# Performance work log

Measured on AMD Instinct MI355X. Metric: run time of the kernel, lower is better.

Reference implementation:

```python
import jax, jax.numpy as jnp
import numpy as np

N, E, B = 100000, 160000, 4096
F_NODE, F_EDGE, H, DEPTH = 133, 14, 512, 5


def setup_inputs() -> dict:
    key = jax.random.key(0)
    ks = jax.random.split(key, 12)
    P = E // 2
    src = jax.random.randint(ks[0], (P,), 0, N)
    dst = jax.random.randint(ks[1], (P,), 0, N)
    # interleave so edge 2k = (src,dst) and 2k+1 = (dst,src); reverse of e is e^1
    row = jnp.stack([src, dst], axis=1).reshape(-1)
    col = jnp.stack([dst, src], axis=1).reshape(-1)
    edge_index = jnp.stack([row, col], axis=0)
    x = jax.random.normal(ks[2], (N, F_NODE), jnp.float32)
    edge_attr = jax.random.normal(ks[3], (E, F_EDGE), jnp.float32)
    batch = jnp.sort(jax.random.randint(ks[4], (N,), 0, B))
    s = 0.05
    return dict(
        x=x, edge_attr=edge_attr, edge_index=edge_index, batch=batch,
        W_init=jax.random.normal(ks[5], (F_NODE + F_EDGE, H), jnp.float32) * s,
        b_init=jnp.zeros((H,), jnp.float32),
        W_conv=jax.random.normal(ks[6], (DEPTH, H, H), jnp.float32) * s,
        b_conv=jnp.zeros((DEPTH, H), jnp.float32),
        W_e2n=jax.random.normal(ks[7], (F_NODE + H, H), jnp.float32) * s,
        b_e2n=jnp.zeros((H,), jnp.float32),
        W_ffn1=jax.random.normal(ks[8], (H, H), jnp.float32) * s,
        b_ffn1=jnp.zeros((H,), jnp.float32),
        W_ffn2=jax.random.normal(ks[9], (H, 1), jnp.float32) * s,
        b_ffn2=jnp.zeros((1,), jnp.float32),
    )


def _dmpnn_conv(h, row, col, rev, W, b):
    # node aggregation: sum incoming edge messages at each destination node
    a = jax.ops.segment_sum(h, col, num_segments=N)          # [N, H]
    # new edge message for (i->j): agg at i minus reverse-edge message (j->i)
    msg = a[row] - h[rev]                                    # [E, H]
    return a, msg @ W + b


def reference(x, edge_attr, edge_index, batch, W_init, b_init, W_conv, b_conv,
              W_e2n, b_e2n, W_ffn1, b_ffn1, W_ffn2, b_ffn2):
    row, col = edge_index[0], edge_index[1]
    rev = jnp.arange(E) ^ 1
    # edge_init: relu(Linear(cat([x[row], edge_attr])))
    h0 = jax.nn.relu(jnp.concatenate([x[row], edge_attr], axis=1) @ W_init + b_init)
    h = h0
    for l in range(DEPTH):
        _, h = _dmpnn_conv(h, row, col, rev, W_conv[l], b_conv[l])
        h = jax.nn.relu(h + h0)  # residual to h0, relu (dropout=0, eval mode)
    # final conv reuses last layer (l == DEPTH-1 as in the torch loop variable)
    s_node, _ = _dmpnn_conv(h, row, col, rev, W_conv[DEPTH - 1], b_conv[DEPTH - 1])
    q = jnp.concatenate([x, s_node], axis=1)                 # [N, F_NODE+H]
    hn = jax.nn.relu(q @ W_e2n + b_e2n)                      # [N, H]
    pooled = jax.ops.segment_sum(hn, batch, num_segments=B)  # global_add_pool [B, H]
    out = jax.nn.relu(pooled @ W_ffn1 + b_ffn1) @ W_ffn2 + b_ffn2
    return out.squeeze(-1)                                   # [B]
```

## Files before the change

### kernel.cpp

```cpp
#include <hip/hip_runtime.h>

typedef _Float16 f16;
typedef _Float16 f16x8 __attribute__((ext_vector_type(8)));
typedef float f32x4 __attribute__((ext_vector_type(4)));

#define NN 100000
#define NE 160000
#define NB 4096
#define HD 512

#define O_H8    0UL
#define O_SCE   81920000UL
#define O_SHR   87040000UL
#define O_WT    141440000UL
#define O_OFF   145437696UL
#define O_EID   145837712UL
#define WS_NEEDED 146477712UL
#define V_POOL  0UL
#define V_PH    8388608UL
#define V_T1    12582912UL
#define V_CNT   16777216UL
#define V_FILL  17177232UL
#define V_BSUM  17577248UL

__global__ void zero16(ulong2* __restrict__ p, long n) {
  long i = (long)blockIdx.x * 256 + threadIdx.x;
  if (i < n) p[i] = ulong2{0UL, 0UL};
}
__global__ void diag(float* __restrict__ out, int n, float v) {
  int i = blockIdx.x * 256 + threadIdx.x;
  if (i < n) out[i] = v;
}

__global__ void transcast(const float* __restrict__ src, f16* __restrict__ dst,
                          int Kreal, int Kpad) {
  int id = blockIdx.x * 256 + threadIdx.x;
  if (id >= 512 * Kpad) return;
  int n = id / Kpad, k = id % Kpad;
  dst[((k >> 5) * 512 + n) * 32 + (k & 31)] =
      (k < Kreal) ? (f16)src[(size_t)k * 512 + n] : (f16)0.f;
}

__global__ void countK(const int* __restrict__ col, int* __restrict__ cnt) {
  int e = blockIdx.x * 256 + threadIdx.x;
  if (e < NE) atomicAdd(&cnt[col[e]], 1);
}
__global__ __launch_bounds__(1024) void scanA(const int* __restrict__ cnt,
                                              int* __restrict__ incl, int* __restrict__ bsum) {
  __shared__ int s[1024];
  int i = blockIdx.x * 1024 + threadIdx.x;
  s[threadIdx.x] = (i < NN) ? cnt[i] : 0;
  __syncthreads();
  for (int d = 1; d < 1024; d <<= 1) {
    int t = (threadIdx.x >= d) ? s[threadIdx.x - d] : 0;
    __syncthreads();
    s[threadIdx.x] += t;
    __syncthreads();
  }
  if (i < NN) incl[i] = s[threadIdx.x];
  if (threadIdx.x == 1023) bsum[blockIdx.x] = s[1023];
}
__global__ void scanB(int* bsum, int nb) {
  if (threadIdx.x == 0 && blockIdx.x == 0) {
    int run = 0;
    for (int i = 0; i < nb; ++i) { int t = bsum[i]; bsum[i] = run; run += t; }
  }
}
__global__ __launch_bounds__(1024) void scanC(const int* __restrict__ cnt,
                                              int* __restrict__ incl_fill,
                                              const int* __restrict__ bsum,
                                              int* __restrict__ off) {
  int i = blockIdx.x * 1024 + threadIdx.x;
  if (i >= NN) return;
  int g = incl_fill[i] + bsum[blockIdx.x];
  off[i + 1] = g;
  incl_fill[i] = g - cnt[i];
  if (i == 0) off[0] = 0;
}
__global__ void scatterK(const int* __restrict__ col, int* __restrict__ fill,
                         int* __restrict__ eid) {
  int e = blockIdx.x * 256 + threadIdx.x;
  if (e >= NE) return;
  int p = atomicAdd(&fill[col[e]], 1);
  eid[p] = e;
}

template<int C0>
__global__ __launch_bounds__(256, 4)
void msgk(const char* __restrict__ z8, const float* __restrict__ sce,
          const int* __restrict__ off, const int* __restrict__ eid,
          char* __restrict__ msgq, float* __restrict__ scm) {
  int tid = threadIdx.x, wid = tid >> 6, lane = tid & 63;
  int n = blockIdx.x * 4 + wid;
  int s0 = off[n], s1 = off[n + 1];
  int g = lane >> 4;
  float a[4] = {0.f, 0.f, 0.f, 0.f};
  for (int p = s0; p < s1; ++p) {
    int e = eid[p];
    float sc = sce[e * 8 + (C0 >> 6) + g];
    unsigned u = *reinterpret_cast<const unsigned*>(z8 + (size_t)e * 512 + C0 + lane * 4);
    #pragma unroll
    for (int b = 0; b < 4; ++b)
      a[b] += (float)(char)((u >> (8 * b)) & 0xff) * sc;
  }
  for (int p = s0; p < s1; ++p) {
    int e = eid[p];
    int f = e ^ 1;
    float sc = sce[e * 8 + (C0 >> 6) + g];
    unsigned u = *reinterpret_cast<const unsigned*>(z8 + (size_t)e * 512 + C0 + lane * 4);
    float mv[4]; float m = 0.f;
    #pragma unroll
    for (int b = 0; b < 4; ++b) {
      mv[b] = a[b] - (float)(char)((u >> (8 * b)) & 0xff) * sc;
      m = fmaxf(m, fabsf(mv[b]));
    }
    #pragma unroll
    for (int d = 1; d < 16; d <<= 1) m = fmaxf(m, __shfl_xor(m, d));
    float s2 = (m > 0.f) ? m / 127.f : 1.f;
    if ((lane & 15) == 0) scm[f * 4 + g] = s2;
    unsigned q = 0;
    #pragma unroll
    for (int b = 0; b < 4; ++b) {
      int qi = __float2int_rn(mv[b] / s2);
      qi = min(127, max(-127, qi));
      q |= ((unsigned)(unsigned char)(char)qi) << (8 * b);
    }
    *reinterpret_cast<unsigned*>(msgq + (size_t)f * 256 + lane * 4) = q;
  }
}

__global__ __launch_bounds__(256, 4)
void tker(const char* __restrict__ h8, const float* __restrict__ sce,
          const int* __restrict__ off, const int* __restrict__ eid,
          char* __restrict__ nb8, float* __restrict__ scn) {
  int tid = threadIdx.x, wid = tid >> 6, lane = tid & 63;
  int n = blockIdx.x * 4 + wid;
  int s0 = off[n], s1 = off[n + 1];
  int g = lane >> 3;
  float a[8] = {0.f,0.f,0.f,0.f,0.f,0.f,0.f,0.f};
  for (int p = s0; p < s1; ++p) {
    int e = eid[p];
    float sc = sce[e * 8 + g];
    uint2 u = *reinterpret_cast<const uint2*>(h8 + (size_t)e * 512 + lane * 8);
    #pragma unroll
    for (int b = 0; b < 4; ++b) {
      a[b]     += (float)((u.x >> (8 * b)) & 0xff) * sc;
      a[4 + b] += (float)((u.y >> (8 * b)) & 0xff) * sc;
    }
  }
  float m = 0.f;
  #pragma unroll
  for (int j = 0; j < 8; ++j) m = fmaxf(m, a[j]);
  #pragma unroll
  for (int d = 1; d < 8; d <<= 1) m = fmaxf(m, __shfl_xor(m, d));
  float s2 = (m > 0.f) ? m / 255.f : 1.f;
  if ((lane & 7) == 0) scn[n * 8 + g] = s2;
  unsigned lo = 0, hi = 0;
  #pragma unroll
  for (int b = 0; b < 4; ++b) {
    int q0 = __float2int_rn(a[b] / s2);     q0 = min(255, max(0, q0));
    int q1 = __float2int_rn(a[4 + b] / s2); q1 = min(255, max(0, q1));
    lo |= ((unsigned)q0) << (8 * b);
    hi |= ((unsigned)q1) << (8 * b);
  }
  *reinterpret_cast<uint2*>(nb8 + (size_t)n * 512 + lane * 8) = uint2{lo, hi};
}

static __device__ __forceinline__ void stageB512(const f16* __restrict__ wsrc,
                                                 f16* __restrict__ Bs, int tid) {
  #pragma unroll
  for (int j = 0; j < 4; ++j) {
    int u = tid * 4 + j;
    *reinterpret_cast<f16x8*>(&Bs[(u >> 2) * 40 + (u & 3) * 8]) =
        *reinterpret_cast<const f16x8*>(&wsrc[u * 8]);
  }
}
template<int AS>
static __device__ __forceinline__ void mstep8(const f16* __restrict__ As,
                                              const f16* __restrict__ Bs,
                                              f32x4 acc[2][8], int wm, int wn,
                                              int fr, int fg, int ko) {
  f16x8 af[2];
  #pragma unroll
  for (int mf = 0; mf < 2; ++mf)
    af[mf] = *reinterpret_cast<const f16x8*>(&As[(wm + mf * 16 + fr) * AS + ko + fg * 8]);
  #pragma unroll
  for (int nf = 0; nf < 8; ++nf) {
    f16x8 bf = *reinterpret_cast<const f16x8*>(&Bs[(wn + nf * 16 + fr) * 40 + fg * 8]);
    #pragma unroll
    for (int mf = 0; mf < 2; ++mf)
      acc[mf][nf] = __builtin_amdgcn_mfma_f32_16x16x32_f16(af[mf], bf, acc[mf][nf], 0, 0, 0);
  }
}

__global__ __launch_bounds__(512, 1)
void zk(char* __restrict__ h8, float* __restrict__ sce, const f16* __restrict__ wst) {
  __shared__ f16 As[64 * 520];
  __shared__ f16 Bs[2][512 * 40];
  const int tid = threadIdx.x, lane = tid & 63, wid = tid >> 6;
  const int fr = lane & 15, fg = lane >> 4;
  const int wm = (wid >> 2) * 32, wn = (wid & 3) * 128;
  const int e0 = blockIdx.x * 64;

  {
    int r = tid >> 3, s = tid & 7, kb = s * 64;
    float sc = sce[(size_t)(e0 + r) * 8 + s];
    const int4* src = reinterpret_cast<const int4*>(h8 + (size_t)(e0 + r) * 512 + kb);
    #pragma unroll
    for (int j = 0; j < 4; ++j) {
      int4 w = src[j];
      unsigned vv[4] = {(unsigned)w.x, (unsigned)w.y, (unsigned)w.z, (unsigned)w.w};
      f16 tmp[16];
      #pragma unroll
      for (int q = 0; q < 4; ++q)
        #pragma unroll
        for (int b = 0; b < 4; ++b)
          tmp[q * 4 + b] = (f16)((float)((vv[q] >> (8 * b)) & 0xff) * sc);
      *reinterpret_cast<f16x8*>(&As[r * 520 + kb + j * 16])     = *reinterpret_cast<f16x8*>(&tmp[0]);
      *reinterpret_cast<f16x8*>(&As[r * 520 + kb + j * 16 + 8]) = *reinterpret_cast<f16x8*>(&tmp[8]);
    }
  }
  stageB512(wst, Bs[0], tid);
  __syncthreads();
  f32x4 acc[2][8] = {};
  for (int step = 0; step < 16; ++step) {
    const int cur = step & 1;
    f16x8 pf[4];
    if (step < 15) {
      const f16* wsrc = wst + (size_t)(step + 1) * 16384;
      #pragma unroll
      for (int j = 0; j < 4; ++j)
        pf[j] = *reinterpret_cast<const f16x8*>(&wsrc[(size_t)(tid * 4 + j) * 8]);
    }
    mstep8<520>(As, Bs[cur], acc, wm, wn, fr, fg, step * 32);
    if (step < 15) {
      #pragma unroll
      for (int j = 0; j < 4; ++j) {
        int u = tid * 4 + j;
        *reinterpret_cast<f16x8*>(&Bs[cur ^ 1][(u >> 2) * 40 + (u & 3) * 8]) = pf[j];
      }
    }
    __syncthreads();
  }
  float scA[2][4], scB[2][4];
  #pragma unroll
  for (int mf = 0; mf < 2; ++mf)
    #pragma unroll
    for (int i = 0; i < 4; ++i) {
      float mA = 0.f, mB = 0.f;
      #pragma unroll
      for (int nf = 0; nf < 4; ++nf) mA = fmaxf(mA, fabsf(acc[mf][nf][i]));
      #pragma unroll
      for (int nf = 4; nf < 8; ++nf) mB = fmaxf(mB, fabsf(acc[mf][nf][i]));
      #pragma unroll
      for (int d = 1; d < 16; d <<= 1) {
        mA = fmaxf(mA, __shfl_xor(mA, d));
        mB = fmaxf(mB, __shfl_xor(mB, d));
      }
      scA[mf][i] = (mA > 0.f) ? mA / 127.f : 1.f;
      scB[mf][i] = (mB > 0.f) ? mB / 127.f : 1.f;
      if (fr == 0) {
        int r = wm + mf * 16 + fg * 4 + i;
        sce[(size_t)(e0 + r) * 8 + (wn >> 6)]     = scA[mf][i];
        sce[(size_t)(e0 + r) * 8 + (wn >> 6) + 1] = scB[mf][i];
      }
    }
  char* q8 = (char*)&Bs[0][0];
  #pragma unroll
  for (int mf = 0; mf < 2; ++mf)
    #pragma unroll
    for (int nf = 0; nf < 8; ++nf) {
      int c = wn + nf * 16 + fr;
      #pragma unroll
      for (int i = 0; i < 4; ++i) {
        int r = wm + mf * 16 + fg * 4 + i;
        float s = (nf < 4) ? scA[mf][i] : scB[mf][i];
        int q = __float2int_rn(acc[mf][nf][i] / s);
        q8[r * 512 + c] = (char)min(127, max(-127, q));
      }
    }
  __syncthreads();
  { int4* dst = reinterpret_cast<int4*>(h8 + (size_t)e0 * 512);
    const int4* s4 = reinterpret_cast<const int4*>(q8);
    #pragma unroll
    for (int j = 0; j < 4; ++j) dst[tid * 4 + j] = s4[tid * 4 + j]; }
}

template<int MODE>
__global__ __launch_bounds__(512, 2)
void convup(const float* __restrict__ x, const float* __restrict__ ea,
            const int* __restrict__ row, const f16* __restrict__ wi,
            const float* __restrict__ bi, const float* __restrict__ bc,
            char* __restrict__ h8, float* __restrict__ sce,
            const char* __restrict__ msgq, const float* __restrict__ scm,
            int c0) {
  __shared__ f16 As[64 * 168];
  __shared__ f16 Bs[2][256 * 40];
  __shared__ char m8s[64 * 256];
  __shared__ float scmL[64 * 4];
  const int tid = threadIdx.x, lane = tid & 63, wid = tid >> 6;
  const int fr = lane & 15, fg = lane >> 4;
  const int wm = (wid >> 2) * 32, wn = (wid & 3) * 64;
  const int e0 = blockIdx.x * 64;

  {
    int r = tid >> 3, s = tid & 7;
    int rid = row[e0 + r];
    for (int k = s; k < 133; k += 8) As[r * 168 + k] = (f16)x[(size_t)rid * 133 + k];
    for (int k = 133 + s; k < 147; k += 8) As[r * 168 + k] = (f16)ea[(size_t)(e0 + r) * 14 + (k - 133)];
    for (int k = 147 + s; k < 160; k += 8) As[r * 168 + k] = (f16)0.f;
    if (MODE == 1) {
      const int4* ms = reinterpret_cast<const int4*>(msgq + (size_t)(e0 + r) * 256 + s * 32);
      int4* md = reinterpret_cast<int4*>(m8s + r * 256 + s * 32);
      md[0] = ms[0]; md[1] = ms[1];
      if (s < 4) scmL[r * 4 + s] = scm[(size_t)(e0 + r) * 4 + s];
    }
  }
  {
    #pragma unroll
    for (int j = 0; j < 2; ++j) {
      int u = tid * 2 + j;
      *reinterpret_cast<f16x8*>(&Bs[0][(u >> 2) * 40 + (u & 3) * 8]) =
          *reinterpret_cast<const f16x8*>(&wi[(size_t)c0 * 32 + (size_t)u * 8]);
    }
  }
  __syncthreads();
  f32x4 acc[2][4] = {};
  for (int step = 0; step < 5; ++step) {
    const int cur = step & 1;
    f16x8 pf[2];
    if (step < 4) {
      const f16* wsrc = wi + (size_t)(step + 1) * 16384 + (size_t)c0 * 32;
      #pragma unroll
      for (int j = 0; j < 2; ++j)
        pf[j] = *reinterpret_cast<const f16x8*>(&wsrc[(size_t)(tid * 2 + j) * 8]);
    }
    f16x8 af[2];
    #pragma unroll
    for (int mf = 0; mf < 2; ++mf)
      af[mf] = *reinterpret_cast<const f16x8*>(&As[(wm + mf * 16 + fr) * 168 + step * 32 + fg * 8]);
    #pragma unroll
    for (int nf = 0; nf < 4; ++nf) {
      f16x8 bf = *reinterpret_cast<const f16x8*>(&Bs[cur][(wn + nf * 16 + fr) * 40 + fg * 8]);
      #pragma unroll
      for (int mf = 0; mf < 2; ++mf)
        acc[mf][nf] = __builtin_amdgcn_mfma_f32_16x16x32_f16(af[mf], bf, acc[mf][nf], 0, 0, 0);
    }
    if (step < 4) {
      #pragma unroll
      for (int j = 0; j < 2; ++j) {
        int u = tid * 2 + j;
        *reinterpret_cast<f16x8*>(&Bs[cur ^ 1][(u >> 2) * 40 + (u & 3) * 8]) = pf[j];
      }
    }
    __syncthreads();
  }
  #pragma unroll
  for (int nf = 0; nf < 4; ++nf) {
    int cl = wn + nf * 16 + fr;
    int cg = c0 + cl;
    float bi_ = bi[cg];
    float bc_ = (MODE == 1) ? bc[cg] : 0.f;
    #pragma unroll
    for (int mf = 0; mf < 2; ++mf)
      #pragma unroll
      for (int i = 0; i < 4; ++i) {
        int r = wm + mf * 16 + fg * 4 + i;
        float v = fmaxf(acc[mf][nf][i] + bi_, 0.f);
        if (MODE == 1) {
          float mv = (float)(char)m8s[r * 256 + cl] * scmL[r * 4 + (cl >> 6)];
          v = fmaxf(v + bc_ + mv, 0.f);
        }
        acc[mf][nf][i] = v;
      }
  }
  float sc_[2][4];
  #pragma unroll
  for (int mf = 0; mf < 2; ++mf)
    #pragma unroll
    for (int i = 0; i < 4; ++i) {
      float m = 0.f;
      #pragma unroll
      for (int nf = 0; nf < 4; ++nf) m = fmaxf(m, acc[mf][nf][i]);
      #pragma unroll
      for (int d = 1; d < 16; d <<= 1) m = fmaxf(m, __shfl_xor(m, d));
      sc_[mf][i] = (m > 0.f) ? m / 255.f : 1.f;
      if (fr == 0)
        sce[(size_t)(e0 + wm + mf * 16 + fg * 4 + i) * 8 + (c0 >> 6) + (wn >> 6)] = sc_[mf][i];
    }
  __syncthreads();
  #pragma unroll
  for (int mf = 0; mf < 2; ++mf)
    #pragma unroll
    for (int nf = 0; nf < 4; ++nf) {
      int cl = wn + nf * 16 + fr;
      #pragma unroll
      for (int i = 0; i < 4; ++i) {
        int r = wm + mf * 16 + fg * 4 + i;
        int q = __float2int_rn(acc[mf][nf][i] / sc_[mf][i]);
        m8s[r * 256 + cl] = (char)(unsigned char)min(255, max(0, q));
      }
    }
  __syncthreads();
  { int r = tid >> 3, s = tid & 7;
    int4* dst = reinterpret_cast<int4*>(h8 + (size_t)(e0 + r) * 512 + c0 + s * 32);
    const int4* sp = reinterpret_cast<const int4*>(m8s + r * 256 + s * 32);
    dst[0] = sp[0]; dst[1] = sp[1]; }
}

__global__ __launch_bounds__(512, 1)
void e2n(const float* __restrict__ x, const char* __restrict__ nb8,
         const float* __restrict__ scn, const f16* __restrict__ wex,
         const f16* __restrict__ wes, const float* __restrict__ be,
         const int* __restrict__ batch, float* __restrict__ pooled) {
  __shared__ f16 As[64 * 520];
  __shared__ f16 Bs[2][512 * 40];
  __shared__ int bat[64];
  const int tid = threadIdx.x, lane = tid & 63, wid = tid >> 6;
  const int fr = lane & 15, fg = lane >> 4;
  const int wm = (wid >> 2) * 32, wn = (wid & 3) * 128;
  const int n0 = blockIdx.x * 64;
  if (tid < 64) { int nn = n0 + tid; bat[tid] = (nn < NN) ? batch[nn] : 0; }
  {
    int r = tid >> 3, s = tid & 7;
    int nid = min(n0 + r, NN - 1);
    for (int k = s; k < 133; k += 8) As[r * 168 + k] = (f16)x[(size_t)nid * 133 + k];
    for (int k = 133 + s; k < 160; k += 8) As[r * 168 + k] = (f16)0.f;
  }
  stageB512(wex, Bs[0], tid);
  __syncthreads();
  f32x4 acc[2][8] = {};
  for (int step = 0; step < 5; ++step) {
    const int cur = step & 1;
    f16x8 pf[4];
    if (step < 4) {
      const f16* wsrc = wex + (size_t)(step + 1) * 16384;
      #pragma unroll
      for (int j = 0; j < 4; ++j)
        pf[j] = *reinterpret_cast<const f16x8*>(&wsrc[(size_t)(tid * 4 + j) * 8]);
    }
    mstep8<168>(As, Bs[cur], acc, wm, wn, fr, fg, step * 32);
    if (step < 4) {
      #pragma unroll
      for (int j = 0; j < 4; ++j) {
        int u = tid * 4 + j;
        *reinterpret_cast<f16x8*>(&Bs[cur ^ 1][(u >> 2) * 40 + (u & 3) * 8]) = pf[j];
      }
    }
    __syncthreads();
  }
  {
    int r = tid >> 3, s = tid & 7, kb = s * 64;
    int nid = min(n0 + r, NN - 1);
    float sc = scn[(size_t)nid * 8 + s];
    const int4* src = reinterpret_cast<const int4*>(nb8 + (size_t)nid * 512 + kb);
    #pragma unroll
    for (int j = 0; j < 4; ++j) {
      int4 w = src[j];
      unsigned vv[4] = {(unsigned)w.x, (unsigned)w.y, (unsigned)w.z, (unsigned)w.w};
      f16 tmp[16];
      #pragma unroll
      for (int q = 0; q < 4; ++q)
        #pragma unroll
        for (int b = 0; b < 4; ++b)
          tmp[q * 4 + b] = (f16)((float)((vv[q] >> (8 * b)) & 0xff) * sc);
      *reinterpret_cast<f16x8*>(&As[r * 520 + kb + j * 16])     = *reinterpret_cast<f16x8*>(&tmp[0]);
      *reinterpret_cast<f16x8*>(&As[r * 520 + kb + j * 16 + 8]) = *reinterpret_cast<f16x8*>(&tmp[8]);
    }
  }
  stageB512(wes, Bs[0], tid);
  __syncthreads();
  for (int step = 0; step < 16; ++step) {
    const int cur = step & 1;
    f16x8 pf[4];
    if (step < 15) {
      const f16* wsrc = wes + (size_t)(step + 1) * 16384;
      #pragma unroll
      for (int j = 0; j < 4; ++j)
        pf[j] = *reinterpret_cast<const f16x8*>(&wsrc[(size_t)(tid * 4 + j) * 8]);
    }
    mstep8<520>(As, Bs[cur], acc, wm, wn, fr, fg, step * 32);
    if (step < 15) {
      #pragma unroll
      for (int j = 0; j < 4; ++j) {
        int u = tid * 4 + j;
        *reinterpret_cast<f16x8*>(&Bs[cur ^ 1][(u >> 2) * 40 + (u & 3) * 8]) = pf[j];
      }
    }
    __syncthreads();
  }
  #pragma unroll
  for (int nf = 0; nf < 8; ++nf) {
    int c = wn + nf * 16 + fr;
    float b_ = be[c];
    #pragma unroll
    for (int mf = 0; mf < 2; ++mf)
      #pragma unroll
      for (int i = 0; i < 4; ++i) {
        int rl = wm + mf * 16 + fg * 4 + i;
        As[rl * 520 + c] = (f16)fmaxf(acc[mf][nf][i] + b_, 0.f);
      }
  }
  __syncthreads();
  {
    const int c = tid;
    float s = 0.f;
    int pb = bat[0];
    #pragma unroll 1
    for (int r = 0; r < 64; ++r) {
      if (n0 + r >= NN) break;
      int b = bat[r];
      if (b != pb) {
        atomicAdd(&pooled[(size_t)pb * 512 + c], s);
        s = 0.f; pb = b;
      }
      s += (float)As[r * 520 + c];
    }
    atomicAdd(&pooled[(size_t)pb * 512 + c], s);
  }
}

__global__ __launch_bounds__(512, 1)
void ffn1(const f16* __restrict__ ph, const f16* __restrict__ wf,
          const float* __restrict__ b1, f16* __restrict__ t1) {
  __shared__ f16 As[64 * 520];
  __shared__ f16 Bs[2][512 * 40];
  const int tid = threadIdx.x, lane = tid & 63, wid = tid >> 6;
  const int fr = lane & 15, fg = lane >> 4;
  const int wm = (wid >> 2) * 32, wn = (wid & 3) * 128;
  const int n0 = blockIdx.x * 64;
  { int r = tid >> 3, hs = (tid & 7) * 64;
    #pragma unroll
    for (int j = 0; j < 8; ++j)
      *reinterpret_cast<f16x8*>(&As[r * 520 + hs + j * 8]) =
          *reinterpret_cast<const f16x8*>(&ph[(size_t)(n0 + r) * 512 + hs + j * 8]); }
  stageB512(wf, Bs[0], tid);
  __syncthreads();
  f32x4 acc[2][8] = {};
  for (int step = 0; step < 16; ++step) {
    const int cur = step & 1;
    f16x8 pf[4];
    if (step < 15) {
      const f16* wsrc = wf + (size_t)(step + 1) * 16384;
      #pragma unroll
      for (int j = 0; j < 4; ++j)
        pf[j] = *reinterpret_cast<const f16x8*>(&wsrc[(size_t)(tid * 4 + j) * 8]);
    }
    mstep8<520>(As, Bs[cur], acc, wm, wn, fr, fg, step * 32);
    if (step < 15) {
      #pragma unroll
      for (int j = 0; j < 4; ++j) {
        int u = tid * 4 + j;
        *reinterpret_cast<f16x8*>(&Bs[cur ^ 1][(u >> 2) * 40 + (u & 3) * 8]) = pf[j];
      }
    }
    __syncthreads();
  }
  f16* q16 = As;
  #pragma unroll
  for (int nf = 0; nf < 8; ++nf) {
    int c = wn + nf * 16 + fr;
    float b_ = b1[c];
    #pragma unroll
    for (int mf = 0; mf < 2; ++mf)
      #pragma unroll
      for (int i = 0; i < 4; ++i) {
        int r = wm + mf * 16 + fg * 4 + i;
        q16[r * 512 + c] = (f16)fmaxf(acc[mf][nf][i] + b_, 0.f);
      }
  }
  __syncthreads();
  #pragma unroll
  for (int j = 0; j < 8; ++j)
    *reinterpret_cast<f16x8*>(&t1[(size_t)n0 * 512 + tid * 64 + j * 8]) =
        *reinterpret_cast<const f16x8*>(&q16[tid * 64 + j * 8]);
}

__global__ void cast_ph(const float* __restrict__ pooled, f16* __restrict__ ph) {
  int id = blockIdx.x * 256 + threadIdx.x;
  if (id >= NB * 64) return;
  int k = id * 8;
  f16 v[8];
  #pragma unroll
  for (int i = 0; i < 8; ++i) v[i] = (f16)pooled[k + i];
  *reinterpret_cast<f16x8*>(&ph[k]) = *reinterpret_cast<f16x8*>(&v[0]);
}

__global__ void final_out(const f16* __restrict__ t, const float* __restrict__ W2,
                          const float* __restrict__ b2, float* __restrict__ out) {
  int id = blockIdx.x * 256 + threadIdx.x;
  if (id >= NB * 64) return;
  int b = id >> 6, lane = id & 63;
  f16x8 v = *reinterpret_cast<const f16x8*>(&t[(size_t)b * HD + lane * 8]);
  float s = 0.f;
  #pragma unroll
  for (int i = 0; i < 8; ++i) s += (float)v[i] * W2[lane * 8 + i];
  #pragma unroll
  for (int o = 32; o > 0; o >>= 1) s += __shfl_down(s, o);
  if (lane == 0) out[b] = s + b2[0];
}

extern "C" void kernel_launch(void* const* d_in, const int* in_sizes, int n_in,
                              void* d_out, int out_size, void* d_ws, size_t ws_size,
                              hipStream_t stream) {
  const float* x      = (const float*)d_in[0];
  const float* ea     = (const float*)d_in[1];
  const int*   ei     = (const int*)d_in[2];
  const int*   batch  = (const int*)d_in[3];
  const float* W_init = (const float*)d_in[4];
  const float* b_init = (const float*)d_in[5];
  const float* W_conv = (const float*)d_in[6];
  const float* b_conv = (const float*)d_in[7];
  const float* W_e2n  = (const float*)d_in[8];
  const float* b_e2n  = (const float*)d_in[9];
  const float* W_ffn1 = (const float*)d_in[10];
  const float* b_ffn1 = (const float*)d_in[11];
  const float* W_ffn2 = (const float*)d_in[12];
  const float* b_ffn2 = (const float*)d_in[13];
  const int* row = ei;
  const int* col = ei + NE;
  float* out = (float*)d_out;

  if (ws_size < WS_NEEDED) {
    diag<<<(out_size + 255) / 256, 256, 0, stream>>>(out, out_size, (float)(ws_size >> 20));
    return;
  }

  char* ws = (char*)d_ws;
  char*  h8   = ws + O_H8;
  float* sce  = (float*)(ws + O_SCE);
  char*  msgq = ws + O_SHR;
  float* scm  = (float*)(ws + O_SHR + 40960000UL);
  char*  nb8  = ws + O_SHR;
  float* scn  = (float*)(ws + O_SHR + 51200000UL);
  f16*   wt   = (f16*)(ws + O_WT);
  int*   off  = (int*)(ws + O_OFF);
  int*   eid  = (int*)(ws + O_EID);
  float* pooled = (float*)(ws + V_POOL);
  f16*   ph   = (f16*)(ws + V_PH);
  f16*   t1   = (f16*)(ws + V_T1);
  int*   cnt  = (int*)(ws + V_CNT);
  int*   fill = (int*)(ws + V_FILL);
  int*   bsum = (int*)(ws + V_BSUM);

  f16* wi  = wt;
  f16* wc  = wi + 160 * 512;
  f16* wex = wc + 5 * 512 * 512;
  f16* wes = wex + 160 * 512;
  f16* wf1 = wes + 512 * 512;

  transcast<<<(512 * 160 + 255) / 256, 256, 0, stream>>>(W_init, wi, 147, 160);
  for (int l = 0; l < 5; ++l)
    transcast<<<(512 * 512 + 255) / 256, 256, 0, stream>>>(
        W_conv + (size_t)l * 262144, wc + (size_t)l * 262144, 512, 512);
  transcast<<<(512 * 160 + 255) / 256, 256, 0, stream>>>(W_e2n, wex, 133, 160);
  transcast<<<(512 * 512 + 255) / 256, 256, 0, stream>>>(W_e2n + 133 * 512, wes, 512, 512);
  transcast<<<(512 * 512 + 255) / 256, 256, 0, stream>>>(W_ffn1, wf1, 512, 512);

  zero16<<<(25000 + 255) / 256, 256, 0, stream>>>((ulong2*)cnt, 25000);
  countK<<<(NE + 255) / 256, 256, 0, stream>>>(col, cnt);
  scanA<<<98, 1024, 0, stream>>>(cnt, fill, bsum);
  scanB<<<1, 64, 0, stream>>>(bsum, 98);
  scanC<<<98, 1024, 0, stream>>>(cnt, fill, bsum, off);
  scatterK<<<(NE + 255) / 256, 256, 0, stream>>>(col, fill, eid);

  convup<0><<<2500, 512, 0, stream>>>(x, ea, row, wi, b_init, nullptr,
                                      h8, sce, nullptr, nullptr, 0);
  convup<0><<<2500, 512, 0, stream>>>(x, ea, row, wi, b_init, nullptr,
                                      h8, sce, nullptr, nullptr, 256);
  for (int l = 0; l < 5; ++l) {
    zk<<<2500, 512, 0, stream>>>(h8, sce, wc + (size_t)l * 262144);
    msgk<0><<<25000, 256, 0, stream>>>(h8, sce, off, eid, msgq, scm);
    convup<1><<<2500, 512, 0, stream>>>(x, ea, row, wi, b_init, b_conv + l * 512,
                                        h8, sce, msgq, scm, 0);
    msgk<256><<<25000, 256, 0, stream>>>(h8, sce, off, eid, msgq, scm);
    convup<1><<<2500, 512, 0, stream>>>(x, ea, row, wi, b_init, b_conv + l * 512,
                                        h8, sce, msgq, scm, 256);
  }
  tker<<<25000, 256, 0, stream>>>(h8, sce, off, eid, nb8, scn);
  zero16<<<(524288 + 255) / 256, 256, 0, stream>>>((ulong2*)pooled, 524288);
  e2n<<<1563, 512, 0, stream>>>(x, nb8, scn, wex, wes, b_e2n, batch, pooled);
  cast_ph<<<(NB * 64 + 255) / 256, 256, 0, stream>>>(pooled, ph);
  ffn1<<<64, 512, 0, stream>>>(ph, wf1, b_ffn1, t1);
  final_out<<<(NB * 64 + 255) / 256, 256, 0, stream>>>(t1, W_ffn2, b_ffn2, out);
}
```

Before: 2.864 ms.

## Keep int8 edge tile in LDS and dequantize per step to raise occupancy

```diff
diff --git a/kernel.cpp b/kernel.cpp
--- a/kernel.cpp
+++ b/kernel.cpp
@@ -193,52 +193,50 @@
   }
 }
 
-__global__ __launch_bounds__(512, 1)
+__global__ __launch_bounds__(512, 4)
 void zk(char* __restrict__ h8, float* __restrict__ sce, const f16* __restrict__ wst) {
-  __shared__ f16 As[64 * 520];
-  __shared__ f16 Bs[2][512 * 40];
+  __shared__ unsigned char Asu[64 * 528];
+  __shared__ float scs[64 * 9];
+  __shared__ f16 Bs[512 * 40];
   const int tid = threadIdx.x, lane = tid & 63, wid = tid >> 6;
   const int fr = lane & 15, fg = lane >> 4;
   const int wm = (wid >> 2) * 32, wn = (wid & 3) * 128;
   const int e0 = blockIdx.x * 64;
 
   {
-    int r = tid >> 3, s = tid & 7, kb = s * 64;
-    float sc = sce[(size_t)(e0 + r) * 8 + s];
+    int r = tid >> 3, kb = (tid & 7) * 64;
     const int4* src = reinterpret_cast<const int4*>(h8 + (size_t)(e0 + r) * 512 + kb);
-    #pragma unroll
-    for (int j = 0; j < 4; ++j) {
-      int4 w = src[j];
-      unsigned vv[4] = {(unsigned)w.x, (unsigned)w.y, (unsigned)w.z, (unsigned)w.w};
-      f16 tmp[16];
-      #pragma unroll
-      for (int q = 0; q < 4; ++q)
-        #pragma unroll
-        for (int b = 0; b < 4; ++b)
-          tmp[q * 4 + b] = (f16)((float)((vv[q] >> (8 * b)) & 0xff) * sc);
-      *reinterpret_cast<f16x8*>(&As[r * 520 + kb + j * 16])     = *reinterpret_cast<f16x8*>(&tmp[0]);
-      *reinterpret_cast<f16x8*>(&As[r * 520 + kb + j * 16 + 8]) = *reinterpret_cast<f16x8*>(&tmp[8]);
-    }
-  }
-  stageB512(wst, Bs[0], tid);
+    int4* dst = reinterpret_cast<int4*>(&Asu[r * 528 + kb]);
+    #pragma unroll
+    for (int j = 0; j < 4; ++j) dst[j] = src[j];
+    scs[r * 9 + (tid & 7)] = sce[(size_t)(e0 + r) * 8 + (tid & 7)];
+  }
   __syncthreads();
   f32x4 acc[2][8] = {};
   for (int step = 0; step < 16; ++step) {
-    const int cur = step & 1;
-    f16x8 pf[4];
-    if (step < 15) {
-      const f16* wsrc = wst + (size_t)(step + 1) * 16384;
-      #pragma unroll
-      for (int j = 0; j < 4; ++j)
-        pf[j] = *reinterpret_cast<const f16x8*>(&wsrc[(size_t)(tid * 4 + j) * 8]);
-    }
-    mstep8<520>(As, Bs[cur], acc, wm, wn, fr, fg, step * 32);
-    if (step < 15) {
-      #pragma unroll
-      for (int j = 0; j < 4; ++j) {
-        int u = tid * 4 + j;
-        *reinterpret_cast<f16x8*>(&Bs[cur ^ 1][(u >> 2) * 40 + (u & 3) * 8]) = pf[j];
-      }
+    stageB512(wst + (size_t)step * 16384, Bs, tid);
+    __syncthreads();
+    const int g = step >> 1;
+    f16x8 af[2];
+    #pragma unroll
+    for (int mf = 0; mf < 2; ++mf) {
+      const int row = wm + mf * 16 + fr;
+      const float sa = scs[row * 9 + g];
+      uint2 u = *reinterpret_cast<const uint2*>(&Asu[row * 528 + step * 32 + fg * 8]);
+      f16 t[8];
+      #pragma unroll
+      for (int b = 0; b < 4; ++b) {
+        t[b]     = (f16)((float)((u.x >> (8 * b)) & 0xff) * sa);
+        t[4 + b] = (f16)((float)((u.y >> (8 * b)) & 0xff) * sa);
+      }
+      af[mf] = *reinterpret_cast<f16x8*>(t);
+    }
+    #pragma unroll
+    for (int nf = 0; nf < 8; ++nf) {
+      f16x8 bf = *reinterpret_cast<const f16x8*>(&Bs[(wn + nf * 16 + fr) * 40 + fg * 8]);
+      #pragma unroll
+      for (int mf = 0; mf < 2; ++mf)
+        acc[mf][nf] = __builtin_amdgcn_mfma_f32_16x16x32_f16(af[mf], bf, acc[mf][nf], 0, 0, 0);
     }
     __syncthreads();
   }
@@ -265,7 +263,7 @@
         sce[(size_t)(e0 + r) * 8 + (wn >> 6) + 1] = scB[mf][i];
       }
     }
-  char* q8 = (char*)&Bs[0][0];
+  char* q8 = (char*)&Bs[0];
   #pragma unroll
   for (int mf = 0; mf < 2; ++mf)
     #pragma unroll
```

Result: faster. 2.562 ms (-10.5%).
